# Kernel tuning notes

Hardware: AMD Instinct MI355X
Metric: run time of the kernel (lower is better)

The kernel has to match this reference:

```python
import jax, jax.numpy as jnp
import numpy as np

# dims: S=seq (attention axis 0), B=batch, Din=input_dim, E=adjusted_dim,
# NEXP=num_experts, HID=expert hidden, DOUT=output_dim, NH=heads, TOPK=top_k
S, B, Din, E, NEXP, HID, DOUT, NH, TOPK = 1024, 8, 768, 768, 10, 256, 768, 8, 2
LN_EPS = 1e-5


def setup_inputs() -> dict:
    key = jax.random.key(0)
    ks = jax.random.split(key, 10)
    s = 0.02
    return {
        "x": jax.random.normal(ks[0], (S, B, Din), jnp.float32),
        # input_projection: Linear(Din -> E)
        "Wp": jax.random.normal(ks[1], (E, Din), jnp.float32) * s,
        "bp": jnp.zeros((E,), jnp.float32),
        # MultiheadAttention packed in-proj (3E, E) and out-proj (E, E)
        "Win": jax.random.normal(ks[2], (3 * E, E), jnp.float32) * s,
        "bin_": jnp.zeros((3 * E,), jnp.float32),
        "Wo": jax.random.normal(ks[3], (E, E), jnp.float32) * s,
        "bo": jnp.zeros((E,), jnp.float32),
        # gate: Linear(E -> NEXP)
        "Wg": jax.random.normal(ks[4], (NEXP, E), jnp.float32) * s,
        "bg": jnp.zeros((NEXP,), jnp.float32),
        # experts: NEXP x (Linear(E->HID), ReLU, Linear(HID->DOUT))
        "W1": jax.random.normal(ks[5], (NEXP, E, HID), jnp.float32) * s,
        "b1": jnp.zeros((NEXP, HID), jnp.float32),
        "W2": jax.random.normal(ks[6], (NEXP, HID, DOUT), jnp.float32) * s,
        "b2": jnp.zeros((NEXP, DOUT), jnp.float32),
        # LayerNorm(DOUT)
        "gamma": jnp.ones((DOUT,), jnp.float32),
        "beta": jnp.zeros((DOUT,), jnp.float32),
    }


def reference(x, Wp, bp, Win, bin_, Wo, bo, Wg, bg, W1, b1, W2, b2, gamma, beta):
    hd = E // NH
    # input projection
    h = jnp.einsum('sbd,ed->sbe', x, Wp) + bp  # (S,B,E)
    # self-attention (torch MHA, seq-first, no mask)
    qkv = jnp.einsum('sbe,fe->sbf', h, Win) + bin_  # (S,B,3E)
    q, k, v = jnp.split(qkv, 3, axis=-1)
    q = q.reshape(S, B, NH, hd) * (hd ** -0.5)
    k = k.reshape(S, B, NH, hd)
    v = v.reshape(S, B, NH, hd)
    scores = jnp.einsum('sbhd,tbhd->bhst', q, k)       # (B,NH,S,S)
    attn = jax.nn.softmax(scores, axis=-1)
    ctx = jnp.einsum('bhst,tbhd->sbhd', attn, v).reshape(S, B, E)
    h = jnp.einsum('sbe,fe->sbf', ctx, Wo) + bo        # (S,B,E)
    # top-k gating
    gate_probs = jax.nn.softmax(jnp.einsum('sbe,ne->sbn', h, Wg) + bg, axis=-1)
    top_p, top_i = jax.lax.top_k(gate_probs, TOPK)     # (S,B,TOPK)
    top_p = top_p / jnp.sum(top_p, axis=-1, keepdims=True)
    # combine weights: (S,B,NEXP), zero for unselected experts
    combine = jnp.sum(top_p[..., None] * jax.nn.one_hot(top_i, NEXP, dtype=h.dtype), axis=-2)
    # per-expert MLP, weighted combine (dense dispatch, same math as masked loop)
    eh = jax.nn.relu(jnp.einsum('sbe,neh->sbnh', h, W1) + b1)  # (S,B,NEXP,HID)
    moe = jnp.einsum('sbnh,nho,sbn->sbo', eh, W2, combine) + jnp.einsum('sbn,no->sbo', combine, b2)
    # LayerNorm over DOUT
    mu = jnp.mean(moe, axis=-1, keepdims=True)
    var = jnp.mean((moe - mu) ** 2, axis=-1, keepdims=True)
    moe = (moe - mu) * jax.lax.rsqrt(var + LN_EPS) * gamma + beta
    # attn_weights: head-averaged (B,S,S), then raw .view to (S,B,-1), mean last
    aw = jnp.mean(attn, axis=1)            # (B,S,S)
    aw = aw.reshape(S, B, -1)              # memory reinterpretation as in torch .view
    aw = jnp.mean(aw, axis=-1, keepdims=True)  # (S,B,1)
    return moe * aw, aw
```

## Files before the change

kernel.cpp:

```cpp
#include <hip/hip_runtime.h>
#include <math.h>

#define S_    1024
#define B_    8
#define E_    768
#define NH_   8
#define HD_   96
#define NEXP_ 10
#define HID_  256
#define DOUT_ 768
#define TOK_  (S_*B_)
#define OUT0_ (TOK_*DOUT_)

#define OFF_H1   0
#define OFF_QB   6291456
#define OFF_KB   12582912
#define OFF_VB   18874368
#define OFF_H2   25165824
#define OFF_TW   31457280
#define OFF_INT  (31457280 + 16384)

__global__ void init_counts(int* counts) {
    if (threadIdx.x < 16) counts[threadIdx.x] = 0;
}

template<int MODE>
__global__ __launch_bounds__(256)
void gemm_abt(const float* __restrict__ A, const float* __restrict__ W,
              const float* __restrict__ bias, float* __restrict__ C,
              int M, int N, int K,
              float* __restrict__ qb, float* __restrict__ kb, float* __restrict__ vb)
{
    __shared__ float Ast[16][132];
    __shared__ float Wst[16][132];
    const int tid = threadIdx.x;
    const int tx = tid & 15, ty = tid >> 4;
    const int m0 = blockIdx.x * 128, n0 = blockIdx.y * 128;
    const int lrow = tid >> 2, lkq = tid & 3;

    float acc[8][8];
    #pragma unroll
    for (int i = 0; i < 8; i++)
        #pragma unroll
        for (int j = 0; j < 8; j++) acc[i][j] = 0.f;

    for (int k0 = 0; k0 < K; k0 += 16) {
        #pragma unroll
        for (int h = 0; h < 2; h++) {
            const int row = lrow + h*64;
            const float4 av = *(const float4*)(A + (size_t)(m0+row)*K + k0 + lkq*4);
            Ast[lkq*4+0][row] = av.x; Ast[lkq*4+1][row] = av.y;
            Ast[lkq*4+2][row] = av.z; Ast[lkq*4+3][row] = av.w;
            const float4 wv = *(const float4*)(W + (size_t)(n0+row)*K + k0 + lkq*4);
            Wst[lkq*4+0][row] = wv.x; Wst[lkq*4+1][row] = wv.y;
            Wst[lkq*4+2][row] = wv.z; Wst[lkq*4+3][row] = wv.w;
        }
        __syncthreads();
        #pragma unroll
        for (int kk = 0; kk < 16; kk++) {
            float a[8], w[8];
            *(float4*)&a[0] = *(const float4*)&Ast[kk][ty*4];
            *(float4*)&a[4] = *(const float4*)&Ast[kk][64 + ty*4];
            *(float4*)&w[0] = *(const float4*)&Wst[kk][tx*4];
            *(float4*)&w[4] = *(const float4*)&Wst[kk][64 + tx*4];
            #pragma unroll
            for (int i = 0; i < 8; i++)
                #pragma unroll
                for (int j = 0; j < 8; j++)
                    acc[i][j] = fmaf(a[i], w[j], acc[i][j]);
        }
        __syncthreads();
    }

    const float QS = 0.10206207261596575f;
    #pragma unroll
    for (int i = 0; i < 8; i++) {
        const int m = m0 + ((i < 4) ? (ty*4 + i) : (64 + ty*4 + i - 4));
        #pragma unroll
        for (int jq = 0; jq < 2; jq++) {
            const int nb = n0 + (jq ? (64 + tx*4) : (tx*4));
            const float4 bv = *(const float4*)(bias + nb);
            float4 v;
            v.x = acc[i][jq*4+0] + bv.x;
            v.y = acc[i][jq*4+1] + bv.y;
            v.z = acc[i][jq*4+2] + bv.z;
            v.w = acc[i][jq*4+3] + bv.w;
            if (MODE == 0) {
                *(float4*)(C + (size_t)m*N + nb) = v;
            } else {
                const int s = m >> 3, b = m & 7;
                const int which = nb / E_;
                const int e = nb - which*E_;
                const int h = e / HD_, d = e - h*HD_;
                float* dst = (which == 0) ? qb : (which == 1) ? kb : vb;
                if (which == 0) { v.x *= QS; v.y *= QS; v.z *= QS; v.w *= QS; }
                *(float4*)(dst + ((size_t)((b<<3) + h)*S_ + s)*HD_ + d) = v;
            }
        }
    }
}

__global__ __launch_bounds__(128)
void attn_kernel(const float* __restrict__ qb, const float* __restrict__ kb,
                 const float* __restrict__ vb, float* __restrict__ ctxb)
{
    __shared__ float Ks[64][96];
    __shared__ float Vs[64][96];
    const int tid = threadIdx.x;
    const int bh = blockIdx.y;
    const int srow = blockIdx.x * 128 + tid;
    const float* qp = qb + ((size_t)bh*S_ + srow)*HD_;
    const float* kbase = kb + (size_t)bh*S_*HD_;
    const float* vbase = vb + (size_t)bh*S_*HD_;

    float q[96], cx[96];
    #pragma unroll
    for (int i = 0; i < 24; i++) *(float4*)&q[i*4] = *(const float4*)(qp + i*4);
    #pragma unroll
    for (int i = 0; i < 96; i++) cx[i] = 0.f;
    float l = 0.f;

    for (int t0 = 0; t0 < S_; t0 += 64) {
        __syncthreads();
        for (int lin = tid; lin < 64*24; lin += 128) {
            const int r = lin / 24, c = lin % 24;
            *(float4*)&Ks[r][c*4] = *(const float4*)(kbase + (size_t)(t0+r)*HD_ + c*4);
            *(float4*)&Vs[r][c*4] = *(const float4*)(vbase + (size_t)(t0+r)*HD_ + c*4);
        }
        __syncthreads();
        for (int tt = 0; tt < 64; tt++) {
            float s = 0.f;
            #pragma unroll
            for (int i = 0; i < 24; i++) {
                const float4 kv = *(const float4*)&Ks[tt][i*4];
                s = fmaf(q[i*4+0], kv.x, s); s = fmaf(q[i*4+1], kv.y, s);
                s = fmaf(q[i*4+2], kv.z, s); s = fmaf(q[i*4+3], kv.w, s);
            }
            const float p = __expf(s);
            l += p;
            #pragma unroll
            for (int i = 0; i < 24; i++) {
                const float4 vv = *(const float4*)&Vs[tt][i*4];
                cx[i*4+0] = fmaf(p, vv.x, cx[i*4+0]);
                cx[i*4+1] = fmaf(p, vv.y, cx[i*4+1]);
                cx[i*4+2] = fmaf(p, vv.z, cx[i*4+2]);
                cx[i*4+3] = fmaf(p, vv.w, cx[i*4+3]);
            }
        }
    }
    const float inv = 1.f / l;
    const int b = bh >> 3, h = bh & 7;
    float* op = ctxb + ((size_t)srow*B_ + b)*E_ + h*HD_;
    #pragma unroll
    for (int i = 0; i < 24; i++) {
        float4 o;
        o.x = cx[i*4+0]*inv; o.y = cx[i*4+1]*inv;
        o.z = cx[i*4+2]*inv; o.w = cx[i*4+3]*inv;
        *(float4*)(op + i*4) = o;
    }
}

__global__ __launch_bounds__(256)
void gate_kernel(const float* __restrict__ h2, const float* __restrict__ Wg,
                 const float* __restrict__ bg, int* __restrict__ tix,
                 float* __restrict__ tw, int* __restrict__ counts)
{
    const int lane = threadIdx.x & 63;
    const int tok = blockIdx.x*4 + (threadIdx.x >> 6);
    const float* hr = h2 + (size_t)tok*E_;
    float part[NEXP_];
    #pragma unroll
    for (int n = 0; n < NEXP_; n++) part[n] = 0.f;
    for (int i = 0; i < 12; i++) {
        const float xv = hr[i*64 + lane];
        #pragma unroll
        for (int n = 0; n < NEXP_; n++)
            part[n] = fmaf(xv, Wg[n*E_ + i*64 + lane], part[n]);
    }
    #pragma unroll
    for (int n = 0; n < NEXP_; n++) {
        float v = part[n];
        for (int off = 32; off > 0; off >>= 1) v += __shfl_xor(v, off);
        part[n] = v;
    }
    if (lane == 0) {
        float lg[NEXP_];
        #pragma unroll
        for (int n = 0; n < NEXP_; n++) lg[n] = part[n] + bg[n];
        int i1 = 0; float l1 = lg[0];
        #pragma unroll
        for (int n = 1; n < NEXP_; n++) if (lg[n] > l1) { l1 = lg[n]; i1 = n; }
        int i2 = -1; float l2 = -1e30f;
        #pragma unroll
        for (int n = 0; n < NEXP_; n++) if (n != i1 && lg[n] > l2) { l2 = lg[n]; i2 = n; }
        const float p = __expf(l2 - l1);
        const float w1 = 1.f / (1.f + p);
        tix[tok*2]   = i1; tix[tok*2+1] = i2;
        tw[tok*2]    = w1; tw[tok*2+1]  = 1.f - w1;
        atomicAdd(&counts[i1], 1);
        atomicAdd(&counts[i2], 1);
    }
}

__global__ void scan_kernel(const int* __restrict__ counts, int* __restrict__ offsets,
                            int* __restrict__ cursor) {
    if (threadIdx.x == 0) {
        int run = 0;
        for (int e = 0; e < NEXP_; e++) { offsets[e] = run; cursor[e] = run; run += counts[e]; }
    }
}

__global__ __launch_bounds__(256)
void scatter_kernel(const int* __restrict__ tix, int* __restrict__ cursor,
                    int* __restrict__ elist) {
    const int tok = blockIdx.x*256 + threadIdx.x;
    #pragma unroll
    for (int slot = 0; slot < 2; slot++) {
        const int e = tix[tok*2 + slot];
        const int pos = atomicAdd(&cursor[e], 1);
        elist[pos] = tok*2 + slot;
    }
}

__global__ __launch_bounds__(256)
void expert_mlp1(const float* __restrict__ h2, const float* __restrict__ W1,
                 const float* __restrict__ b1, const int* __restrict__ offsets,
                 const int* __restrict__ counts, const int* __restrict__ elist,
                 float* __restrict__ eh)
{
    const int e = blockIdx.z;
    const int cnt = counts[e];
    const int mt = blockIdx.x;
    if (mt*128 >= cnt) return;
    const int off = offsets[e];
    const int n0 = blockIdx.y * 128;
    __shared__ float Ast[16][132];
    __shared__ float Wst[16][132];
    __shared__ int toks[128];
    const int tid = threadIdx.x;
    const int tx = tid & 15, ty = tid >> 4;
    const int lrow = tid >> 2, lkq = tid & 3;
    if (tid < 128) {
        const int r = mt*128 + tid;
        toks[tid] = (r < cnt) ? (elist[off + r] >> 1) : (elist[off] >> 1);
    }
    __syncthreads();
    const float* W = W1 + (size_t)e*E_*HID_;
    const float* b1e = b1 + (size_t)e*HID_;

    float acc[8][8];
    #pragma unroll
    for (int i = 0; i < 8; i++)
        #pragma unroll
        for (int j = 0; j < 8; j++) acc[i][j] = 0.f;

    for (int k0 = 0; k0 < E_; k0 += 16) {
        #pragma unroll
        for (int h = 0; h < 2; h++) {
            const int row = lrow + h*64;
            const float4 av = *(const float4*)(h2 + (size_t)toks[row]*E_ + k0 + lkq*4);
            Ast[lkq*4+0][row] = av.x; Ast[lkq*4+1][row] = av.y;
            Ast[lkq*4+2][row] = av.z; Ast[lkq*4+3][row] = av.w;
            const int lin = tid + h*256;
            const int kk = lin >> 5, nq = lin & 31;
            *(float4*)&Wst[kk][nq*4] = *(const float4*)(W + (size_t)(k0+kk)*HID_ + n0 + nq*4);
        }
        __syncthreads();
        #pragma unroll
        for (int kk = 0; kk < 16; kk++) {
            float a[8], w[8];
            *(float4*)&a[0] = *(const float4*)&Ast[kk][ty*4];
            *(float4*)&a[4] = *(const float4*)&Ast[kk][64 + ty*4];
            *(float4*)&w[0] = *(const float4*)&Wst[kk][tx*4];
            *(float4*)&w[4] = *(const float4*)&Wst[kk][64 + tx*4];
            #pragma unroll
            for (int i = 0; i < 8; i++)
                #pragma unroll
                for (int j = 0; j < 8; j++)
                    acc[i][j] = fmaf(a[i], w[j], acc[i][j]);
        }
        __syncthreads();
    }
    #pragma unroll
    for (int i = 0; i < 8; i++) {
        const int ri = (i < 4) ? (ty*4 + i) : (64 + ty*4 + i - 4);
        const int r = mt*128 + ri;
        if (r >= cnt) continue;
        const size_t pos = (size_t)(off + r);
        #pragma unroll
        for (int jq = 0; jq < 2; jq++) {
            const int nb = n0 + (jq ? (64 + tx*4) : (tx*4));
            const float4 bv = *(const float4*)(b1e + nb);
            float4 v;
            v.x = fmaxf(acc[i][jq*4+0] + bv.x, 0.f);
            v.y = fmaxf(acc[i][jq*4+1] + bv.y, 0.f);
            v.z = fmaxf(acc[i][jq*4+2] + bv.z, 0.f);
            v.w = fmaxf(acc[i][jq*4+3] + bv.w, 0.f);
            *(float4*)(eh + pos*HID_ + nb) = v;
        }
    }
}

__global__ __launch_bounds__(256)
void expert_mlp2(const float* __restrict__ eh, const float* __restrict__ W2,
                 const float* __restrict__ b2, const float* __restrict__ tw,
                 const int* __restrict__ offsets, const int* __restrict__ counts,
                 const int* __restrict__ elist,
                 float* __restrict__ moe0, float* __restrict__ moe1)
{
    const int e = blockIdx.z;
    const int cnt = counts[e];
    const int mt = blockIdx.x;
    if (mt*128 >= cnt) return;
    const int off = offsets[e];
    const int n0 = blockIdx.y * 128;
    __shared__ float Ast[16][132];
    __shared__ float Wst[16][132];
    __shared__ int ents[128];
    __shared__ float tws[128];
    const int tid = threadIdx.x;
    const int tx = tid & 15, ty = tid >> 4;
    const int lrow = tid >> 2, lkq = tid & 3;
    if (tid < 128) {
        const int r = mt*128 + tid;
        const int ent = (r < cnt) ? elist[off + r] : elist[off];
        ents[tid] = ent;
        tws[tid] = tw[ent];
    }
    __syncthreads();
    const float* W = W2 + (size_t)e*HID_*DOUT_;
    const float* b2e = b2 + (size_t)e*DOUT_;

    float acc[8][8];
    #pragma unroll
    for (int i = 0; i < 8; i++)
        #pragma unroll
        for (int j = 0; j < 8; j++) acc[i][j] = 0.f;

    for (int k0 = 0; k0 < HID_; k0 += 16) {
        #pragma unroll
        for (int h = 0; h < 2; h++) {
            const int row = lrow + h*64;
            const size_t pos = (size_t)(off + ((mt*128 + row < cnt) ? (mt*128 + row) : 0));
            const float4 av = *(const float4*)(eh + pos*HID_ + k0 + lkq*4);
            Ast[lkq*4+0][row] = av.x; Ast[lkq*4+1][row] = av.y;
            Ast[lkq*4+2][row] = av.z; Ast[lkq*4+3][row] = av.w;
            const int lin = tid + h*256;
            const int kk = lin >> 5, nq = lin & 31;
            *(float4*)&Wst[kk][nq*4] = *(const float4*)(W + (size_t)(k0+kk)*DOUT_ + n0 + nq*4);
        }
        __syncthreads();
        #pragma unroll
        for (int kk = 0; kk < 16; kk++) {
            float a[8], w[8];
            *(float4*)&a[0] = *(const float4*)&Ast[kk][ty*4];
            *(float4*)&a[4] = *(const float4*)&Ast[kk][64 + ty*4];
            *(float4*)&w[0] = *(const float4*)&Wst[kk][tx*4];
            *(float4*)&w[4] = *(const float4*)&Wst[kk][64 + tx*4];
            #pragma unroll
            for (int i = 0; i < 8; i++)
                #pragma unroll
                for (int j = 0; j < 8; j++)
                    acc[i][j] = fmaf(a[i], w[j], acc[i][j]);
        }
        __syncthreads();
    }
    #pragma unroll
    for (int i = 0; i < 8; i++) {
        const int ri = (i < 4) ? (ty*4 + i) : (64 + ty*4 + i - 4);
        const int r = mt*128 + ri;
        if (r >= cnt) continue;
        const int ent = ents[ri];
        const int tok = ent >> 1;
        const float wt = tws[ri];
        float* dst = (ent & 1) ? moe1 : moe0;
        #pragma unroll
        for (int jq = 0; jq < 2; jq++) {
            const int nb = n0 + (jq ? (64 + tx*4) : (tx*4));
            const float4 bv = *(const float4*)(b2e + nb);
            float4 v;
            v.x = (acc[i][jq*4+0] + bv.x) * wt;
            v.y = (acc[i][jq*4+1] + bv.y) * wt;
            v.z = (acc[i][jq*4+2] + bv.z) * wt;
            v.w = (acc[i][jq*4+3] + bv.w) * wt;
            *(float4*)(dst + (size_t)tok*DOUT_ + nb) = v;
        }
    }
}

__global__ __launch_bounds__(256)
void ln_kernel(const float* __restrict__ m0b, const float* __restrict__ m1b,
               const float* __restrict__ gamma, const float* __restrict__ beta,
               float* __restrict__ out)
{
    __shared__ float red[8];
    const int tk = blockIdx.x;
    const int tid = threadIdx.x;
    float v[3];
    float s = 0.f;
    #pragma unroll
    for (int j = 0; j < 3; j++) {
        const int c = tid + j*256;
        v[j] = m0b[(size_t)tk*DOUT_ + c] + m1b[(size_t)tk*DOUT_ + c];
        s += v[j];
    }
    for (int off = 32; off > 0; off >>= 1) s += __shfl_xor(s, off);
    if ((tid & 63) == 0) red[tid >> 6] = s;
    __syncthreads();
    const float mu = (red[0]+red[1]+red[2]+red[3]) * (1.f/768.f);
    float s2 = 0.f;
    #pragma unroll
    for (int j = 0; j < 3; j++) { const float d = v[j] - mu; s2 += d*d; }
    for (int off = 32; off > 0; off >>= 1) s2 += __shfl_xor(s2, off);
    if ((tid & 63) == 0) red[4 + (tid >> 6)] = s2;
    __syncthreads();
    const float var = (red[4]+red[5]+red[6]+red[7]) * (1.f/768.f);
    const float rs = rsqrtf(var + 1e-5f);
    const float AW = 0.0009765625f;
    #pragma unroll
    for (int j = 0; j < 3; j++) {
        const int c = tid + j*256;
        out[(size_t)tk*DOUT_ + c] = ((v[j] - mu)*rs*gamma[c] + beta[c]) * AW;
    }
    if (tid == 0) out[OUT0_ + tk] = AW;
}

extern "C" void kernel_launch(void* const* d_in, const int* in_sizes, int n_in,
                              void* d_out, int out_size, void* d_ws, size_t ws_size,
                              hipStream_t stream)
{
    const float* x    = (const float*)d_in[0];
    const float* Wp   = (const float*)d_in[1];
    const float* bp   = (const float*)d_in[2];
    const float* Win  = (const float*)d_in[3];
    const float* binp = (const float*)d_in[4];
    const float* Wo   = (const float*)d_in[5];
    const float* bo   = (const float*)d_in[6];
    const float* Wg   = (const float*)d_in[7];
    const float* bg   = (const float*)d_in[8];
    const float* W1   = (const float*)d_in[9];
    const float* b1   = (const float*)d_in[10];
    const float* W2   = (const float*)d_in[11];
    const float* b2   = (const float*)d_in[12];
    const float* gamma= (const float*)d_in[13];
    const float* beta = (const float*)d_in[14];
    float* out = (float*)d_out;

    float* wsf  = (float*)d_ws;
    float* h1   = wsf + OFF_H1;
    float* qb   = wsf + OFF_QB;
    float* kb   = wsf + OFF_KB;
    float* vb   = wsf + OFF_VB;
    float* h2   = wsf + OFF_H2;
    float* ctx  = h1;
    float* eh   = qb;
    float* moe0 = kb;
    float* moe1 = vb;
    float* tw   = wsf + OFF_TW;
    int* ib     = (int*)(wsf + OFF_INT);
    int* tix    = ib;
    int* elist  = ib + 16384;
    int* counts = ib + 32768;
    int* offs   = ib + 32768 + 16;
    int* cursor = ib + 32768 + 32;

    init_counts<<<1, 64, 0, stream>>>(counts);
    gemm_abt<0><<<dim3(64, 6), 256, 0, stream>>>(x, Wp, bp, h1, TOK_, E_, E_, nullptr, nullptr, nullptr);
    gemm_abt<1><<<dim3(64, 18), 256, 0, stream>>>(h1, Win, binp, nullptr, TOK_, 3*E_, E_, qb, kb, vb);
    attn_kernel<<<dim3(8, 64), 128, 0, stream>>>(qb, kb, vb, ctx);
    gemm_abt<0><<<dim3(64, 6), 256, 0, stream>>>(ctx, Wo, bo, h2, TOK_, E_, E_, nullptr, nullptr, nullptr);
    gate_kernel<<<2048, 256, 0, stream>>>(h2, Wg, bg, tix, tw, counts);
    scan_kernel<<<1, 64, 0, stream>>>(counts, offs, cursor);
    scatter_kernel<<<32, 256, 0, stream>>>(tix, cursor, elist);
    expert_mlp1<<<dim3(64, 2, NEXP_), 256, 0, stream>>>(h2, W1, b1, offs, counts, elist, eh);
    expert_mlp2<<<dim3(64, 6, NEXP_), 256, 0, stream>>>(eh, W2, b2, tw, offs, counts, elist, moe0, moe1);
    ln_kernel<<<TOK_, 256, 0, stream>>>(moe0, moe1, gamma, beta, out);
    (void)in_sizes; (void)n_in; (void)out_size; (void)ws_size;
}
```

Before: 2.166 ms.

## Prefetch GEMM tiles into registers and split attention keys across half-waves

```diff
diff --git a/kernel.cpp b/kernel.cpp
--- a/kernel.cpp
+++ b/kernel.cpp
@@ -20,6 +20,11 @@
 #define OFF_TW   31457280
 #define OFF_INT  (31457280 + 16384)
 
+__device__ __forceinline__ void gload_lds16(const float* g, float* l) {
+    __builtin_amdgcn_global_load_lds((const __attribute__((address_space(1))) void*)(g),
+                                     (__attribute__((address_space(3))) void*)(l), 16, 0, 0);
+}
+
 __global__ void init_counts(int* counts) {
     if (threadIdx.x < 16) counts[threadIdx.x] = 0;
 }
@@ -38,24 +43,40 @@
     const int m0 = blockIdx.x * 128, n0 = blockIdx.y * 128;
     const int lrow = tid >> 2, lkq = tid & 3;
 
+    const float* Ab0 = A + (size_t)(m0 + lrow)*K + lkq*4;
+    const float* Ab1 = Ab0 + (size_t)64*K;
+    const float* Wb0 = W + (size_t)(n0 + lrow)*K + lkq*4;
+    const float* Wb1 = Wb0 + (size_t)64*K;
+
+    float4 pa0 = *(const float4*)Ab0;
+    float4 pa1 = *(const float4*)Ab1;
+    float4 pw0 = *(const float4*)Wb0;
+    float4 pw1 = *(const float4*)Wb1;
+
     float acc[8][8];
     #pragma unroll
     for (int i = 0; i < 8; i++)
         #pragma unroll
         for (int j = 0; j < 8; j++) acc[i][j] = 0.f;
 
-    for (int k0 = 0; k0 < K; k0 += 16) {
-        #pragma unroll
-        for (int h = 0; h < 2; h++) {
-            const int row = lrow + h*64;
-            const float4 av = *(const float4*)(A + (size_t)(m0+row)*K + k0 + lkq*4);
-            Ast[lkq*4+0][row] = av.x; Ast[lkq*4+1][row] = av.y;
-            Ast[lkq*4+2][row] = av.z; Ast[lkq*4+3][row] = av.w;
-            const float4 wv = *(const float4*)(W + (size_t)(n0+row)*K + k0 + lkq*4);
-            Wst[lkq*4+0][row] = wv.x; Wst[lkq*4+1][row] = wv.y;
-            Wst[lkq*4+2][row] = wv.z; Wst[lkq*4+3][row] = wv.w;
-        }
-        __syncthreads();
+    for (int k0 = 0;;) {
+        Ast[lkq*4+0][lrow]    = pa0.x; Ast[lkq*4+1][lrow]    = pa0.y;
+        Ast[lkq*4+2][lrow]    = pa0.z; Ast[lkq*4+3][lrow]    = pa0.w;
+        Ast[lkq*4+0][lrow+64] = pa1.x; Ast[lkq*4+1][lrow+64] = pa1.y;
+        Ast[lkq*4+2][lrow+64] = pa1.z; Ast[lkq*4+3][lrow+64] = pa1.w;
+        Wst[lkq*4+0][lrow]    = pw0.x; Wst[lkq*4+1][lrow]    = pw0.y;
+        Wst[lkq*4+2][lrow]    = pw0.z; Wst[lkq*4+3][lrow]    = pw0.w;
+        Wst[lkq*4+0][lrow+64] = pw1.x; Wst[lkq*4+1][lrow+64] = pw1.y;
+        Wst[lkq*4+2][lrow+64] = pw1.z; Wst[lkq*4+3][lrow+64] = pw1.w;
+        __syncthreads();
+        k0 += 16;
+        const bool more = (k0 < K);
+        if (more) {
+            pa0 = *(const float4*)(Ab0 + k0);
+            pa1 = *(const float4*)(Ab1 + k0);
+            pw0 = *(const float4*)(Wb0 + k0);
+            pw1 = *(const float4*)(Wb1 + k0);
+        }
         #pragma unroll
         for (int kk = 0; kk < 16; kk++) {
             float a[8], w[8];
@@ -70,6 +91,7 @@
                     acc[i][j] = fmaf(a[i], w[j], acc[i][j]);
         }
         __syncthreads();
+        if (!more) break;
     }
 
     const float QS = 0.10206207261596575f;
@@ -100,15 +122,19 @@
     }
 }
 
-__global__ __launch_bounds__(128)
+__global__ __launch_bounds__(256, 2)
 void attn_kernel(const float* __restrict__ qb, const float* __restrict__ kb,
                  const float* __restrict__ vb, float* __restrict__ ctxb)
 {
-    __shared__ float Ks[64][96];
-    __shared__ float Vs[64][96];
+    __shared__ float Ks[64*96];
+    __shared__ float Vs[64*96];
     const int tid = threadIdx.x;
+    const int wave = tid >> 6;
+    const int lane = tid & 63;
+    const int part = lane >> 5;
+    const int rloc = wave*32 + (lane & 31);
     const int bh = blockIdx.y;
-    const int srow = blockIdx.x * 128 + tid;
+    const int srow = blockIdx.x*128 + rloc;
     const float* qp = qb + ((size_t)bh*S_ + srow)*HD_;
     const float* kbase = kb + (size_t)bh*S_*HD_;
     const float* vbase = vb + (size_t)bh*S_*HD_;
@@ -121,42 +147,54 @@
     float l = 0.f;
 
     for (int t0 = 0; t0 < S_; t0 += 64) {
-        __syncthreads();
-        for (int lin = tid; lin < 64*24; lin += 128) {
-            const int r = lin / 24, c = lin % 24;
-            *(float4*)&Ks[r][c*4] = *(const float4*)(kbase + (size_t)(t0+r)*HD_ + c*4);
-            *(float4*)&Vs[r][c*4] = *(const float4*)(vbase + (size_t)(t0+r)*HD_ + c*4);
-        }
-        __syncthreads();
-        for (int tt = 0; tt < 64; tt++) {
-            float s = 0.f;
+        #pragma unroll
+        for (int j = 0; j < 6; j++) {
+            const int f = j*256 + tid;
+            const int r = f / 24, c = f % 24;
+            gload_lds16(kbase + (size_t)(t0+r)*HD_ + c*4, &Ks[f*4]);
+            gload_lds16(vbase + (size_t)(t0+r)*HD_ + c*4, &Vs[f*4]);
+        }
+        __syncthreads();
+        const int tb = part*32;
+        for (int tt2 = 0; tt2 < 32; tt2++) {
+            const float* kr = &Ks[(size_t)(tb+tt2)*96];
+            float sacc[4] = {0.f, 0.f, 0.f, 0.f};
             #pragma unroll
             for (int i = 0; i < 24; i++) {
-                const float4 kv = *(const float4*)&Ks[tt][i*4];
-                s = fmaf(q[i*4+0], kv.x, s); s = fmaf(q[i*4+1], kv.y, s);
-                s = fmaf(q[i*4+2], kv.z, s); s = fmaf(q[i*4+3], kv.w, s);
+                const float4 kv = *(const float4*)(kr + i*4);
+                float sv = sacc[i & 3];
+                sv = fmaf(q[i*4+0], kv.x, sv); sv = fmaf(q[i*4+1], kv.y, sv);
+                sv = fmaf(q[i*4+2], kv.z, sv); sv = fmaf(q[i*4+3], kv.w, sv);
+                sacc[i & 3] = sv;
             }
-            const float p = __expf(s);
+            const float p = __expf((sacc[0]+sacc[1])+(sacc[2]+sacc[3]));
             l += p;
+            const float* vr = &Vs[(size_t)(tb+tt2)*96];
             #pragma unroll
             for (int i = 0; i < 24; i++) {
-                const float4 vv = *(const float4*)&Vs[tt][i*4];
+                const float4 vv = *(const float4*)(vr + i*4);
                 cx[i*4+0] = fmaf(p, vv.x, cx[i*4+0]);
                 cx[i*4+1] = fmaf(p, vv.y, cx[i*4+1]);
                 cx[i*4+2] = fmaf(p, vv.z, cx[i*4+2]);
                 cx[i*4+3] = fmaf(p, vv.w, cx[i*4+3]);
             }
         }
-    }
-    const float inv = 1.f / l;
-    const int b = bh >> 3, h = bh & 7;
-    float* op = ctxb + ((size_t)srow*B_ + b)*E_ + h*HD_;
-    #pragma unroll
-    for (int i = 0; i < 24; i++) {
-        float4 o;
-        o.x = cx[i*4+0]*inv; o.y = cx[i*4+1]*inv;
-        o.z = cx[i*4+2]*inv; o.w = cx[i*4+3]*inv;
-        *(float4*)(op + i*4) = o;
+        __syncthreads();
+    }
+    l += __shfl_xor(l, 32);
+    #pragma unroll
+    for (int i = 0; i < 96; i++) cx[i] += __shfl_xor(cx[i], 32);
+    if (part == 0) {
+        const float inv = 1.f / l;
+        const int b = bh >> 3, h = bh & 7;
+        float* op = ctxb + ((size_t)srow*B_ + b)*E_ + h*HD_;
+        #pragma unroll
+        for (int i = 0; i < 24; i++) {
+            float4 o;
+            o.x = cx[i*4+0]*inv; o.y = cx[i*4+1]*inv;
+            o.z = cx[i*4+2]*inv; o.w = cx[i*4+3]*inv;
+            *(float4*)(op + i*4) = o;
+        }
     }
 }
 
@@ -248,24 +286,40 @@
     const float* W = W1 + (size_t)e*E_*HID_;
     const float* b1e = b1 + (size_t)e*HID_;
 
+    const int kkA = tid >> 5, nqA = tid & 31;
+    const int kkB = kkA + 8;
+    const float* A0 = h2 + (size_t)toks[lrow]*E_ + lkq*4;
+    const float* A1 = h2 + (size_t)toks[lrow+64]*E_ + lkq*4;
+    const float* Wq0 = W + (size_t)kkA*HID_ + n0 + nqA*4;
+    const float* Wq1 = W + (size_t)kkB*HID_ + n0 + nqA*4;
+
+    float4 pa0 = *(const float4*)A0;
+    float4 pa1 = *(const float4*)A1;
+    float4 pw0 = *(const float4*)Wq0;
+    float4 pw1 = *(const float4*)Wq1;
+
     float acc[8][8];
     #pragma unroll
     for (int i = 0; i < 8; i++)
         #pragma unroll
         for (int j = 0; j < 8; j++) acc[i][j] = 0.f;
 
-    for (int k0 = 0; k0 < E_; k0 += 16) {
-        #pragma unroll
-        for (int h = 0; h < 2; h++) {
-            const int row = lrow + h*64;
-            const float4 av = *(const float4*)(h2 + (size_t)toks[row]*E_ + k0 + lkq*4);
-            Ast[lkq*4+0][row] = av.x; Ast[lkq*4+1][row] = av.y;
-            Ast[lkq*4+2][row] = av.z; Ast[lkq*4+3][row] = av.w;
-            const int lin = tid + h*256;
-            const int kk = lin >> 5, nq = lin & 31;
-            *(float4*)&Wst[kk][nq*4] = *(const float4*)(W + (size_t)(k0+kk)*HID_ + n0 + nq*4);
-        }
-        __syncthreads();
+    for (int k0 = 0;;) {
+        Ast[lkq*4+0][lrow]    = pa0.x; Ast[lkq*4+1][lrow]    = pa0.y;
+        Ast[lkq*4+2][lrow]    = pa0.z; Ast[lkq*4+3][lrow]    = pa0.w;
+        Ast[lkq*4+0][lrow+64] = pa1.x; Ast[lkq*4+1][lrow+64] = pa1.y;
+        Ast[lkq*4+2][lrow+64] = pa1.z; Ast[lkq*4+3][lrow+64] = pa1.w;
+        *(float4*)&Wst[kkA][nqA*4] = pw0;
+        *(float4*)&Wst[kkB][nqA*4] = pw1;
+        __syncthreads();
+        k0 += 16;
+        const bool more = (k0 < E_);
+        if (more) {
+            pa0 = *(const float4*)(A0 + k0);
+            pa1 = *(const float4*)(A1 + k0);
+            pw0 = *(const float4*)(Wq0 + (size_t)k0*HID_);
+            pw1 = *(const float4*)(Wq1 + (size_t)k0*HID_);
+        }
         #pragma unroll
         for (int kk = 0; kk < 16; kk++) {
             float a[8], w[8];
@@ -280,6 +334,7 @@
                     acc[i][j] = fmaf(a[i], w[j], acc[i][j]);
         }
         __syncthreads();
+        if (!more) break;
     }
     #pragma unroll
     for (int i = 0; i < 8; i++) {
@@ -331,25 +386,42 @@
     const float* W = W2 + (size_t)e*HID_*DOUT_;
     const float* b2e = b2 + (size_t)e*DOUT_;
 
+    const int kkA = tid >> 5, nqA = tid & 31;
+    const int kkB = kkA + 8;
+    const size_t posA = (size_t)(off + ((mt*128 + lrow      < cnt) ? (mt*128 + lrow)      : 0));
+    const size_t posB = (size_t)(off + ((mt*128 + lrow + 64 < cnt) ? (mt*128 + lrow + 64) : 0));
+    const float* A0 = eh + posA*HID_ + lkq*4;
+    const float* A1 = eh + posB*HID_ + lkq*4;
+    const float* Wq0 = W + (size_t)kkA*DOUT_ + n0 + nqA*4;
+    const float* Wq1 = W + (size_t)kkB*DOUT_ + n0 + nqA*4;
+
+    float4 pa0 = *(const float4*)A0;
+    float4 pa1 = *(const float4*)A1;
+    float4 pw0 = *(const float4*)Wq0;
+    float4 pw1 = *(const float4*)Wq1;
+
     float acc[8][8];
     #pragma unroll
     for (int i = 0; i < 8; i++)
         #pragma unroll
         for (int j = 0; j < 8; j++) acc[i][j] = 0.f;
 
-    for (int k0 = 0; k0 < HID_; k0 += 16) {
-        #pragma unroll
-        for (int h = 0; h < 2; h++) {
-            const int row = lrow + h*64;
-            const size_t pos = (size_t)(off + ((mt*128 + row < cnt) ? (mt*128 + row) : 0));
-            const float4 av = *(const float4*)(eh + pos*HID_ + k0 + lkq*4);
-            Ast[lkq*4+0][row] = av.x; Ast[lkq*4+1][row] = av.y;
-            Ast[lkq*4+2][row] = av.z; Ast[lkq*4+3][row] = av.w;
-            const int lin = tid + h*256;
-            const int kk = lin >> 5, nq = lin & 31;
-            *(float4*)&Wst[kk][nq*4] = *(const float4*)(W + (size_t)(k0+kk)*DOUT_ + n0 + nq*4);
-        }
-        __syncthreads();
+    for (int k0 = 0;;) {
+        Ast[lkq*4+0][lrow]    = pa0.x; Ast[lkq*4+1][lrow]    = pa0.y;
+        Ast[lkq*4+2][lrow]    = pa0.z; Ast[lkq*4+3][lrow]    = pa0.w;
+        Ast[lkq*4+0][lrow+64] = pa1.x; Ast[lkq*4+1][lrow+64] = pa1.y;
+        Ast[lkq*4+2][lrow+64] = pa1.z; Ast[lkq*4+3][lrow+64] = pa1.w;
+        *(float4*)&Wst[kkA][nqA*4] = pw0;
+        *(float4*)&Wst[kkB][nqA*4] = pw1;
+        __syncthreads();
+        k0 += 16;
+        const bool more = (k0 < HID_);
+        if (more) {
+            pa0 = *(const float4*)(A0 + k0);
+            pa1 = *(const float4*)(A1 + k0);
+            pw0 = *(const float4*)(Wq0 + (size_t)k0*DOUT_);
+            pw1 = *(const float4*)(Wq1 + (size_t)k0*DOUT_);
+        }
         #pragma unroll
         for (int kk = 0; kk < 16; kk++) {
             float a[8], w[8];
@@ -364,6 +436,7 @@
                     acc[i][j] = fmaf(a[i], w[j], acc[i][j]);
         }
         __syncthreads();
+        if (!more) break;
     }
     #pragma unroll
     for (int i = 0; i < 8; i++) {
@@ -467,7 +540,7 @@
     init_counts<<<1, 64, 0, stream>>>(counts);
     gemm_abt<0><<<dim3(64, 6), 256, 0, stream>>>(x, Wp, bp, h1, TOK_, E_, E_, nullptr, nullptr, nullptr);
     gemm_abt<1><<<dim3(64, 18), 256, 0, stream>>>(h1, Win, binp, nullptr, TOK_, 3*E_, E_, qb, kb, vb);
-    attn_kernel<<<dim3(8, 64), 128, 0, stream>>>(qb, kb, vb, ctx);
+    attn_kernel<<<dim3(8, 64), 256, 0, stream>>>(qb, kb, vb, ctx);
     gemm_abt<0><<<dim3(64, 6), 256, 0, stream>>>(ctx, Wo, bo, h2, TOK_, E_, E_, nullptr, nullptr, nullptr);
     gate_kernel<<<2048, 256, 0, stream>>>(h2, Wg, bg, tix, tw, counts);
     scan_kernel<<<1, 64, 0, stream>>>(counts, offs, cursor);
```

Measured after the change: 2.211 ms. 1.02x slower.
